# Performance work log

Hardware: AMD Instinct MI355X
Metric: run time of the kernel (lower is better)

The kernel has to match this reference:

```python
import jax, jax.numpy as jnp
import numpy as np

N, E, D_IN, D_H, D_OUT = 50000, 800000, 128, 128, 40
EPS = 1e-5


def setup_inputs() -> dict:
    key = jax.random.key(0)
    ks = jax.random.split(key, 12)
    x = jax.random.normal(ks[0], (N, D_IN), dtype=jnp.float32)
    edge_index = jax.random.randint(ks[1], (2, E), 0, N, dtype=jnp.int32)
    s = 1.0 / np.sqrt(D_H)
    return {
        "x": x,
        "edge_index": edge_index,
        "W1": jax.random.normal(ks[2], (D_IN, D_H), jnp.float32) * s,
        "b1": jnp.zeros((D_H,), jnp.float32),
        "W2": jax.random.normal(ks[3], (D_H, D_H), jnp.float32) * s,
        "b2": jnp.zeros((D_H,), jnp.float32),
        "g1": jnp.ones((D_H,), jnp.float32),
        "be1": jnp.zeros((D_H,), jnp.float32),
        "g2": jnp.ones((D_H,), jnp.float32),
        "be2": jnp.zeros((D_H,), jnp.float32),
        "g3": jnp.ones((D_H,), jnp.float32),
        "be3": jnp.zeros((D_H,), jnp.float32),
        "Wm": jax.random.normal(ks[4], (D_H, D_OUT), jnp.float32) * s,
        "bm": jnp.zeros((D_OUT,), jnp.float32),
    }


def _gcn_conv(x, W, b, src, dst, dinv):
    # GCNConv: x' = D^{-1/2}(A+I)D^{-1/2} (x W) + b
    xw = x @ W                                   # [N, H]
    coef = dinv[src] * dinv[dst]                 # [E]
    agg = jax.ops.segment_sum(xw[src] * coef[:, None], dst, num_segments=x.shape[0])
    agg = agg + xw * (dinv * dinv)[:, None]      # self-loop term
    return agg + b


def _bn(x, g, b):
    # BatchNorm1d in training mode: biased batch statistics over nodes
    m = jnp.mean(x, axis=0)
    v = jnp.var(x, axis=0)
    return g * (x - m) * jax.lax.rsqrt(v + EPS) + b


def reference(x, edge_index, W1, b1, W2, b2, g1, be1, g2, be2, g3, be3, Wm, bm):
    src, dst = edge_index[0], edge_index[1]
    # degree with self-loops (GCN symmetric normalization, computed on dst/col)
    deg = 1.0 + jax.ops.segment_sum(jnp.ones((E,), jnp.float32), dst, num_segments=N)
    dinv = jax.lax.rsqrt(deg)
    h = _gcn_conv(x, W1, b1, src, dst, dinv)
    h = jax.nn.relu(_bn(h, g1, be1))            # dropout is identity in eval
    h = _gcn_conv(h, W2, b2, src, dst, dinv)
    h = jax.nn.relu(_bn(h, g2, be2))
    h = _bn(h, g3, be3)
    h = h @ Wm + bm
    return jax.nn.log_softmax(h, axis=1)
```

## Files before the change

kernel.cpp:

```cpp
#include <hip/hip_runtime.h>
#include <hip/hip_fp16.h>
#include <math.h>

#define BN_EPS 1e-5f
#define CAP 128

typedef __attribute__((ext_vector_type(8))) short short8;
typedef __attribute__((ext_vector_type(4))) float floatx4;

__device__ inline unsigned short f2bf(float f) {
    union { float f; unsigned u; } x; x.f = f;
    unsigned r = x.u + 0x7fff + ((x.u >> 16) & 1);
    return (unsigned short)(r >> 16);
}
__device__ inline float bf2f(unsigned short h) {
    union { float f; unsigned u; } x; x.u = ((unsigned)h) << 16; return x.f;
}

__device__ inline void bn_sc_sh(float sum, float sumsq, float g, float be, float invN,
                                float& sc, float& sh) {
    float mean = sum * invN;
    float var = sumsq * invN - mean * mean;
    sc = g * rsqrtf(var + BN_EPS);
    sh = be - mean * sc;
}

__device__ inline void pack_one(int idx, const float* W1, const float* W2, const float* Wm,
                                unsigned short* p1, unsigned short* p2, unsigned short* pm) {
    const float* W;
    unsigned short* pack;
    int f, l = idx & 63, t, n, stride, ncols;
    if (idx < 2048) {
        W = W1; pack = p1; f = idx >> 6; t = f >> 3; n = (f & 7) * 16 + (l & 15);
        stride = 128; ncols = 128;
    } else if (idx < 4096) {
        W = W2; pack = p2; f = (idx - 2048) >> 6; t = f >> 3; n = (f & 7) * 16 + (l & 15);
        stride = 128; ncols = 128;
    } else {
        W = Wm; pack = pm; f = (idx - 4096) >> 6; t = f / 3; n = (f % 3) * 16 + (l & 15);
        stride = 40; ncols = 40;
    }
    int q = l >> 4;
    unsigned short* pp = pack + f * 1024 + l * 16;
#pragma unroll
    for (int j = 0; j < 8; ++j) {
        int k = t * 32 + q * 8 + j;
        float v = (n < ncols) ? W[k * stride + n] : 0.f;
        unsigned short hi = f2bf(v);
        float lo = v - bf2f(hi);
        pp[j] = hi;
        pp[8 + j] = f2bf(lo);
    }
}

__global__ __launch_bounds__(256) void k_pre(const float* __restrict__ W1,
                                             const float* __restrict__ W2,
                                             const float* __restrict__ Wm,
                                             unsigned short* __restrict__ p1,
                                             unsigned short* __restrict__ p2,
                                             unsigned short* __restrict__ pm,
                                             int4* __restrict__ zdst, int nz4) {
    if (blockIdx.x < 19) {
        int idx = blockIdx.x * 256 + threadIdx.x;
        if (idx < 4864) pack_one(idx, W1, W2, Wm, p1, p2, pm);
        return;
    }
    int i = (blockIdx.x - 19) * 256 + threadIdx.x;
    if (i < nz4) zdst[i] = make_int4(0, 0, 0, 0);
}

__global__ __launch_bounds__(256) void k_fill(const int* __restrict__ src,
                                              const int* __restrict__ dst, int E,
                                              int* __restrict__ fillc,
                                              unsigned short* __restrict__ col16, int nfill) {
    int b = (int)blockIdx.x;
    int g = b & 7;
    int rank = b >> 3;
    int stride = (nfill >> 3) * 256;
    for (int e = rank * 256 + threadIdx.x; e < E; e += stride) {
        int d = dst[e];
        if ((d & 7) != g) continue;
        int r = atomicAdd(&fillc[d], 1);
        if (r < CAP) col16[(size_t)d * CAP + r] = (unsigned short)src[e];
    }
}

__device__ inline void load_row8(const float* arow, int kbase, float av[8]) {
    float4 a0 = *(const float4*)(arow + kbase);
    float4 a1 = *(const float4*)(arow + kbase + 4);
    av[0] = a0.x; av[1] = a0.y; av[2] = a0.z; av[3] = a0.w;
    av[4] = a1.x; av[5] = a1.y; av[6] = a1.z; av[7] = a1.w;
}
__device__ inline void load_row8(const __half* arow, int kbase, float av[8]) {
    float4 raw = *(const float4*)(arow + kbase);
    const __half2* h = (const __half2*)&raw;
#pragma unroll
    for (int i = 0; i < 4; ++i) {
        float2 f = __half22float2(h[i]);
        av[2 * i] = f.x;
        av[2 * i + 1] = f.y;
    }
}

template <typename T, bool FUSE_BN>
__global__ __launch_bounds__(256) void k_gemm(const T* __restrict__ A,
                                              const unsigned short* __restrict__ packW,
                                              const float* __restrict__ sums,
                                              const float* __restrict__ g,
                                              const float* __restrict__ be, float invN,
                                              const int* __restrict__ fillc,
                                              __half* __restrict__ C16, int M) {
    int lane = threadIdx.x & 63;
    int wv = threadIdx.x >> 6;
    int m0 = ((int)blockIdx.x * 4 + wv) * 16;
    if (m0 >= M) return;
    int row = lane & 15, quad = lane >> 4;

    floatx4 acc[8];
#pragma unroll
    for (int nt = 0; nt < 8; ++nt) acc[nt] = (floatx4){0.f, 0.f, 0.f, 0.f};

    const T* arow = A + (size_t)(m0 + row) * 128;

    float av[4][8];
#pragma unroll
    for (int t = 0; t < 4; ++t) load_row8(arow, t * 32 + quad * 8, av[t]);

#pragma unroll
    for (int t = 0; t < 4; ++t) {
        int kbase = t * 32 + quad * 8;
        if (FUSE_BN) {
#pragma unroll
            for (int j = 0; j < 8; ++j) {
                int c = kbase + j;
                float sc, sh;
                bn_sc_sh(sums[c], sums[128 + c], g[c], be[c], invN, sc, sh);
                av[t][j] = fmaxf(av[t][j] * sc + sh, 0.f);
            }
        }
        short8 ah, al;
#pragma unroll
        for (int j = 0; j < 8; ++j) {
            unsigned short hi = f2bf(av[t][j]);
            ah[j] = (short)hi;
            al[j] = (short)f2bf(av[t][j] - bf2f(hi));
        }
        const unsigned short* wp = packW + (size_t)(t * 8) * 1024 + lane * 16;
#pragma unroll
        for (int nt = 0; nt < 8; ++nt) {
            short8 wh = *(const short8*)wp;
            short8 wl = *(const short8*)(wp + 8);
            wp += 1024;
            acc[nt] = __builtin_amdgcn_mfma_f32_16x16x32_bf16(ah, wh, acc[nt], 0, 0, 0);
            acc[nt] = __builtin_amdgcn_mfma_f32_16x16x32_bf16(al, wh, acc[nt], 0, 0, 0);
            acc[nt] = __builtin_amdgcn_mfma_f32_16x16x32_bf16(ah, wl, acc[nt], 0, 0, 0);
        }
    }

    float d[4];
#pragma unroll
    for (int r = 0; r < 4; ++r) d[r] = rsqrtf(1.f + (float)fillc[m0 + quad * 4 + r]);
#pragma unroll
    for (int nt = 0; nt < 8; ++nt) {
#pragma unroll
        for (int r = 0; r < 4; ++r) {
            C16[(size_t)(m0 + quad * 4 + r) * 128 + nt * 16 + row] =
                __float2half_rn(acc[nt][r] * d[r]);
        }
    }
}

__global__ __launch_bounds__(256) void k_gather(const __half2* __restrict__ y16,
                                                const int* __restrict__ fillc,
                                                const unsigned short* __restrict__ col16,
                                                const float* __restrict__ bias,
                                                __half2* __restrict__ out, int N) {
    int wv = threadIdx.x >> 6;
    int lane = threadIdx.x & 63;
    int n = blockIdx.x * 4 + wv;
    if (n >= N) return;
    float2 acc = __half22float2(y16[(size_t)n * 64 + lane]);
    int degraw = fillc[n];
    int deg = min(degraw, CAP);
    const unsigned short* cb = col16 + (size_t)n * CAP;
    for (int jb = 0; jb < deg; jb += 64) {
        int cnt = min(64, deg - jb);
        int idx = (lane < cnt) ? (int)cb[jb + lane] : 0;
        int jj = 0;
        for (; jj + 8 <= cnt; jj += 8) {
            int s0 = __shfl(idx, jj + 0, 64);
            int s1 = __shfl(idx, jj + 1, 64);
            int s2 = __shfl(idx, jj + 2, 64);
            int s3 = __shfl(idx, jj + 3, 64);
            int s4 = __shfl(idx, jj + 4, 64);
            int s5 = __shfl(idx, jj + 5, 64);
            int s6 = __shfl(idx, jj + 6, 64);
            int s7 = __shfl(idx, jj + 7, 64);
            float2 r0 = __half22float2(y16[(size_t)s0 * 64 + lane]);
            float2 r1 = __half22float2(y16[(size_t)s1 * 64 + lane]);
            float2 r2 = __half22float2(y16[(size_t)s2 * 64 + lane]);
            float2 r3 = __half22float2(y16[(size_t)s3 * 64 + lane]);
            float2 r4 = __half22float2(y16[(size_t)s4 * 64 + lane]);
            float2 r5 = __half22float2(y16[(size_t)s5 * 64 + lane]);
            float2 r6 = __half22float2(y16[(size_t)s6 * 64 + lane]);
            float2 r7 = __half22float2(y16[(size_t)s7 * 64 + lane]);
            acc.x += ((r0.x + r1.x) + (r2.x + r3.x)) + ((r4.x + r5.x) + (r6.x + r7.x));
            acc.y += ((r0.y + r1.y) + (r2.y + r3.y)) + ((r4.y + r5.y) + (r6.y + r7.y));
        }
        for (; jj < cnt; ++jj) {
            int s = __shfl(idx, jj, 64);
            float2 r = __half22float2(y16[(size_t)s * 64 + lane]);
            acc.x += r.x;
            acc.y += r.y;
        }
    }
    float dn = rsqrtf(1.f + (float)degraw);
    float2 b = *(const float2*)&bias[lane << 1];
    float2 o;
    o.x = dn * acc.x + b.x;
    o.y = dn * acc.y + b.y;
    out[(size_t)n * 64 + lane] = __float22half2_rn(o);
}

template <bool TRANSFORM>
__global__ __launch_bounds__(256) void k_stats(const __half2* __restrict__ h, int N,
                                               const float* __restrict__ sums2,
                                               const float* __restrict__ g2,
                                               const float* __restrict__ be2, float invN,
                                               float* __restrict__ stats) {
    int cp = threadIdx.x & 63;
    int rg = threadIdx.x >> 6;
    int rbeg = blockIdx.x * 256;
    int rend = min(rbeg + 256, N);
    float scx = 1.f, shx = 0.f, scy = 1.f, shy = 0.f;
    if (TRANSFORM) {
        int c = cp * 2;
        bn_sc_sh(sums2[c], sums2[128 + c], g2[c], be2[c], invN, scx, shx);
        bn_sc_sh(sums2[c + 1], sums2[128 + c + 1], g2[c + 1], be2[c + 1], invN, scy, shy);
    }
    float sx = 0.f, sy = 0.f, s2x = 0.f, s2y = 0.f;
    for (int r = rbeg + rg; r < rend; r += 4) {
        float2 v = __half22float2(h[(size_t)r * 64 + cp]);
        if (TRANSFORM) {
            v.x = fmaxf(v.x * scx + shx, 0.f);
            v.y = fmaxf(v.y * scy + shy, 0.f);
        }
        sx += v.x; sy += v.y;
        s2x += v.x * v.x; s2y += v.y * v.y;
    }
    __shared__ float ls[4][256];
    ls[0][threadIdx.x] = sx;
    ls[1][threadIdx.x] = sy;
    ls[2][threadIdx.x] = s2x;
    ls[3][threadIdx.x] = s2y;
    __syncthreads();
    if (threadIdx.x < 64) {
        int t = threadIdx.x;
        float a0 = ls[0][t] + ls[0][t + 64] + ls[0][t + 128] + ls[0][t + 192];
        float a1 = ls[1][t] + ls[1][t + 64] + ls[1][t + 128] + ls[1][t + 192];
        float a2 = ls[2][t] + ls[2][t + 64] + ls[2][t + 128] + ls[2][t + 192];
        float a3 = ls[3][t] + ls[3][t + 64] + ls[3][t + 128] + ls[3][t + 192];
        atomicAdd(&stats[2 * t], a0);
        atomicAdd(&stats[2 * t + 1], a1);
        atomicAdd(&stats[128 + 2 * t], a2);
        atomicAdd(&stats[128 + 2 * t + 1], a3);
    }
}

__global__ __launch_bounds__(256) void k_final(const __half* __restrict__ h,
                                               const float* __restrict__ sums2,
                                               const float* __restrict__ g2,
                                               const float* __restrict__ be2,
                                               const float* __restrict__ sums3,
                                               const float* __restrict__ g3,
                                               const float* __restrict__ be3, float invN,
                                               const unsigned short* __restrict__ packWm,
                                               const float* __restrict__ bm,
                                               float* __restrict__ out, int N) {
    int lane = threadIdx.x & 63;
    int wv = threadIdx.x >> 6;
    int m0 = ((int)blockIdx.x * 4 + wv) * 16;
    if (m0 >= N) return;
    int row = lane & 15, quad = lane >> 4;

    floatx4 acc[3];
#pragma unroll
    for (int nt = 0; nt < 3; ++nt) acc[nt] = (floatx4){0.f, 0.f, 0.f, 0.f};

    const __half* arow = h + (size_t)(m0 + row) * 128;

    float av[4][8];
#pragma unroll
    for (int t = 0; t < 4; ++t) load_row8(arow, t * 32 + quad * 8, av[t]);

#pragma unroll
    for (int t = 0; t < 4; ++t) {
        int kbase = t * 32 + quad * 8;
#pragma unroll
        for (int j = 0; j < 8; ++j) {
            int c = kbase + j;
            float sc2, sh2, sc3, sh3;
            bn_sc_sh(sums2[c], sums2[128 + c], g2[c], be2[c], invN, sc2, sh2);
            bn_sc_sh(sums3[c], sums3[128 + c], g3[c], be3[c], invN, sc3, sh3);
            av[t][j] = fmaxf(av[t][j] * sc2 + sh2, 0.f) * sc3 + sh3;
        }
        short8 ah, al;
#pragma unroll
        for (int j = 0; j < 8; ++j) {
            unsigned short hi = f2bf(av[t][j]);
            ah[j] = (short)hi;
            al[j] = (short)f2bf(av[t][j] - bf2f(hi));
        }
        const unsigned short* wp = packWm + (size_t)(t * 3) * 1024 + lane * 16;
#pragma unroll
        for (int nt = 0; nt < 3; ++nt) {
            short8 wh = *(const short8*)wp;
            short8 wl = *(const short8*)(wp + 8);
            wp += 1024;
            acc[nt] = __builtin_amdgcn_mfma_f32_16x16x32_bf16(ah, wh, acc[nt], 0, 0, 0);
            acc[nt] = __builtin_amdgcn_mfma_f32_16x16x32_bf16(al, wh, acc[nt], 0, 0, 0);
            acc[nt] = __builtin_amdgcn_mfma_f32_16x16x32_bf16(ah, wl, acc[nt], 0, 0, 0);
        }
    }

    float bb[3];
#pragma unroll
    for (int nt = 0; nt < 3; ++nt) {
        int col = nt * 16 + row;
        bb[nt] = (col < 40) ? bm[col] : 0.f;
    }
    bool val2 = (row < 8);

#pragma unroll
    for (int r = 0; r < 4; ++r) {
        int m = m0 + quad * 4 + r;
        float v0 = acc[0][r] + bb[0];
        float v1 = acc[1][r] + bb[1];
        float v2 = acc[2][r] + bb[2];
        float mx = fmaxf(v0, v1);
        if (val2) mx = fmaxf(mx, v2);
#pragma unroll
        for (int off = 1; off <= 8; off <<= 1) mx = fmaxf(mx, __shfl_xor(mx, off, 64));
        float s = expf(v0 - mx) + expf(v1 - mx) + (val2 ? expf(v2 - mx) : 0.f);
#pragma unroll
        for (int off = 1; off <= 8; off <<= 1) s += __shfl_xor(s, off, 64);
        float lse = mx + logf(s);
        if (m < N) {
            out[(size_t)m * 40 + row] = v0 - lse;
            out[(size_t)m * 40 + 16 + row] = v1 - lse;
            if (val2) out[(size_t)m * 40 + 32 + row] = v2 - lse;
        }
    }
}

extern "C" void kernel_launch(void* const* d_in, const int* in_sizes, int n_in,
                              void* d_out, int out_size, void* d_ws, size_t ws_size,
                              hipStream_t stream) {
    const float* x   = (const float*)d_in[0];
    const int*   ei  = (const int*)d_in[1];
    const float* W1  = (const float*)d_in[2];
    const float* b1  = (const float*)d_in[3];
    const float* W2  = (const float*)d_in[4];
    const float* b2  = (const float*)d_in[5];
    const float* g1  = (const float*)d_in[6];
    const float* be1 = (const float*)d_in[7];
    const float* g2  = (const float*)d_in[8];
    const float* be2 = (const float*)d_in[9];
    const float* g3  = (const float*)d_in[10];
    const float* be3 = (const float*)d_in[11];
    const float* Wm  = (const float*)d_in[12];
    const float* bm  = (const float*)d_in[13];
    float* out = (float*)d_out;

    int N = in_sizes[0] / 128;
    int E = in_sizes[1] / 2;
    const int* srcs = ei;
    const int* dsts = ei + E;
    float invN = 1.0f / (float)N;

    char* ws = (char*)d_ws;
    size_t off = 0;
    auto alloc = [&](size_t bytes) -> void* {
        void* p = ws + off;
        off += (bytes + 255) & ~(size_t)255;
        return p;
    };
    size_t fill_rounded = (((size_t)N * 4) + 255) & ~(size_t)255;
    int*   fillc   = (int*)alloc((size_t)N * 4);
    float* statsAll= (float*)alloc(3 * 256 * 4);
    float* stats1  = statsAll;
    float* stats2  = statsAll + 256;
    float* stats3  = statsAll + 512;
    unsigned short* col16 = (unsigned short*)alloc((size_t)N * CAP * 2);
    unsigned short* packW1 = (unsigned short*)alloc(32768 * 2);
    unsigned short* packW2 = (unsigned short*)alloc(32768 * 2);
    unsigned short* packWm = (unsigned short*)alloc(12288 * 2);
    __half* y16 = (__half*)alloc((size_t)N * 128 * 2);
    __half* h16 = (__half*)alloc((size_t)N * 128 * 2);
    (void)ws_size; (void)n_in; (void)out_size;

    int nthb = (N + 255) / 256;
    int gatherb = (N + 3) / 4;
    int ngemm = (N + 63) / 64;
    int gfb = (N + 63) / 64;
    const int NFILL = 8192;

    int nz4 = (int)((fill_rounded + 3 * 256 * 4) / 16);
    int zb = (nz4 + 255) / 256;

    k_pre<<<19 + zb, 256, 0, stream>>>(W1, W2, Wm, packW1, packW2, packWm,
                                       (int4*)fillc, nz4);

    k_fill<<<NFILL, 256, 0, stream>>>(srcs, dsts, E, fillc, col16, NFILL);

    k_gemm<float, false><<<ngemm, 256, 0, stream>>>(x, packW1, nullptr, nullptr, nullptr,
                                                    invN, fillc, y16, N);
    k_gather<<<gatherb, 256, 0, stream>>>((const __half2*)y16, fillc, col16, b1,
                                          (__half2*)h16, N);
    k_stats<false><<<nthb, 256, 0, stream>>>((const __half2*)h16, N, nullptr, nullptr, nullptr,
                                             invN, stats1);

    k_gemm<__half, true><<<ngemm, 256, 0, stream>>>(h16, packW2, stats1, g1, be1, invN,
                                                    fillc, y16, N);
    k_gather<<<gatherb, 256, 0, stream>>>((const __half2*)y16, fillc, col16, b2,
                                          (__half2*)h16, N);
    k_stats<false><<<nthb, 256, 0, stream>>>((const __half2*)h16, N, nullptr, nullptr, nullptr,
                                             invN, stats2);

    k_stats<true><<<nthb, 256, 0, stream>>>((const __half2*)h16, N, stats2, g2, be2, invN,
                                            stats3);
    k_final<<<gfb, 256, 0, stream>>>(h16, stats2, g2, be2, stats3, g3, be3, invN, packWm, bm,
                                     out, N);
}
```

Baseline: 322.0 us.

## Merge prep/fill and gather/stats phases into cooperative kernels with grid sync

Replaces separate launches for weight packing plus zeroing plus CSR fill, and for gather plus batch-norm statistics, with persistent cooperative kernels that use grid-wide syncs between phases. The aim is to cut kernel launch gaps and tail effects. In exchange the grid is limited to occupancy-sized persistent blocks, the per-block stats reduction covers more rows, and the fill loses its dst-modulo grouping, which may change atomic contention. Non-cooperative fallbacks are kept.

```diff
diff --git a/kernel.cpp b/kernel.cpp
--- a/kernel.cpp
+++ b/kernel.cpp
@@ -1,6 +1,9 @@
 #include <hip/hip_runtime.h>
+#include <hip/hip_cooperative_groups.h>
 #include <hip/hip_fp16.h>
 #include <math.h>
+
+namespace cg = cooperative_groups;
 
 #define BN_EPS 1e-5f
 #define CAP 128
@@ -53,38 +56,6 @@
     }
 }
 
-__global__ __launch_bounds__(256) void k_pre(const float* __restrict__ W1,
-                                             const float* __restrict__ W2,
-                                             const float* __restrict__ Wm,
-                                             unsigned short* __restrict__ p1,
-                                             unsigned short* __restrict__ p2,
-                                             unsigned short* __restrict__ pm,
-                                             int4* __restrict__ zdst, int nz4) {
-    if (blockIdx.x < 19) {
-        int idx = blockIdx.x * 256 + threadIdx.x;
-        if (idx < 4864) pack_one(idx, W1, W2, Wm, p1, p2, pm);
-        return;
-    }
-    int i = (blockIdx.x - 19) * 256 + threadIdx.x;
-    if (i < nz4) zdst[i] = make_int4(0, 0, 0, 0);
-}
-
-__global__ __launch_bounds__(256) void k_fill(const int* __restrict__ src,
-                                              const int* __restrict__ dst, int E,
-                                              int* __restrict__ fillc,
-                                              unsigned short* __restrict__ col16, int nfill) {
-    int b = (int)blockIdx.x;
-    int g = b & 7;
-    int rank = b >> 3;
-    int stride = (nfill >> 3) * 256;
-    for (int e = rank * 256 + threadIdx.x; e < E; e += stride) {
-        int d = dst[e];
-        if ((d & 7) != g) continue;
-        int r = atomicAdd(&fillc[d], 1);
-        if (r < CAP) col16[(size_t)d * CAP + r] = (unsigned short)src[e];
-    }
-}
-
 __device__ inline void load_row8(const float* arow, int kbase, float av[8]) {
     float4 a0 = *(const float4*)(arow + kbase);
     float4 a1 = *(const float4*)(arow + kbase + 4);
@@ -170,68 +141,67 @@
     }
 }
 
-__global__ __launch_bounds__(256) void k_gather(const __half2* __restrict__ y16,
-                                                const int* __restrict__ fillc,
-                                                const unsigned short* __restrict__ col16,
-                                                const float* __restrict__ bias,
-                                                __half2* __restrict__ out, int N) {
+__device__ void gather_body(const __half2* __restrict__ y16, const int* __restrict__ fillc,
+                            const unsigned short* __restrict__ col16,
+                            const float* __restrict__ bias, __half2* __restrict__ out,
+                            int N) {
     int wv = threadIdx.x >> 6;
     int lane = threadIdx.x & 63;
-    int n = blockIdx.x * 4 + wv;
-    if (n >= N) return;
-    float2 acc = __half22float2(y16[(size_t)n * 64 + lane]);
-    int degraw = fillc[n];
-    int deg = min(degraw, CAP);
-    const unsigned short* cb = col16 + (size_t)n * CAP;
-    for (int jb = 0; jb < deg; jb += 64) {
-        int cnt = min(64, deg - jb);
-        int idx = (lane < cnt) ? (int)cb[jb + lane] : 0;
-        int jj = 0;
-        for (; jj + 8 <= cnt; jj += 8) {
-            int s0 = __shfl(idx, jj + 0, 64);
-            int s1 = __shfl(idx, jj + 1, 64);
-            int s2 = __shfl(idx, jj + 2, 64);
-            int s3 = __shfl(idx, jj + 3, 64);
-            int s4 = __shfl(idx, jj + 4, 64);
-            int s5 = __shfl(idx, jj + 5, 64);
-            int s6 = __shfl(idx, jj + 6, 64);
-            int s7 = __shfl(idx, jj + 7, 64);
-            float2 r0 = __half22float2(y16[(size_t)s0 * 64 + lane]);
-            float2 r1 = __half22float2(y16[(size_t)s1 * 64 + lane]);
-            float2 r2 = __half22float2(y16[(size_t)s2 * 64 + lane]);
-            float2 r3 = __half22float2(y16[(size_t)s3 * 64 + lane]);
-            float2 r4 = __half22float2(y16[(size_t)s4 * 64 + lane]);
-            float2 r5 = __half22float2(y16[(size_t)s5 * 64 + lane]);
-            float2 r6 = __half22float2(y16[(size_t)s6 * 64 + lane]);
-            float2 r7 = __half22float2(y16[(size_t)s7 * 64 + lane]);
-            acc.x += ((r0.x + r1.x) + (r2.x + r3.x)) + ((r4.x + r5.x) + (r6.x + r7.x));
-            acc.y += ((r0.y + r1.y) + (r2.y + r3.y)) + ((r4.y + r5.y) + (r6.y + r7.y));
-        }
-        for (; jj < cnt; ++jj) {
-            int s = __shfl(idx, jj, 64);
-            float2 r = __half22float2(y16[(size_t)s * 64 + lane]);
-            acc.x += r.x;
-            acc.y += r.y;
-        }
-    }
-    float dn = rsqrtf(1.f + (float)degraw);
+    int nwave = (int)gridDim.x * 4;
     float2 b = *(const float2*)&bias[lane << 1];
-    float2 o;
-    o.x = dn * acc.x + b.x;
-    o.y = dn * acc.y + b.y;
-    out[(size_t)n * 64 + lane] = __float22half2_rn(o);
+    for (int n = (int)blockIdx.x * 4 + wv; n < N; n += nwave) {
+        float2 acc = __half22float2(y16[(size_t)n * 64 + lane]);
+        int degraw = fillc[n];
+        int deg = min(degraw, CAP);
+        const unsigned short* cb = col16 + (size_t)n * CAP;
+        for (int jb = 0; jb < deg; jb += 64) {
+            int cnt = min(64, deg - jb);
+            int idx = (lane < cnt) ? (int)cb[jb + lane] : 0;
+            int jj = 0;
+            for (; jj + 8 <= cnt; jj += 8) {
+                int s0 = __shfl(idx, jj + 0, 64);
+                int s1 = __shfl(idx, jj + 1, 64);
+                int s2 = __shfl(idx, jj + 2, 64);
+                int s3 = __shfl(idx, jj + 3, 64);
+                int s4 = __shfl(idx, jj + 4, 64);
+                int s5 = __shfl(idx, jj + 5, 64);
+                int s6 = __shfl(idx, jj + 6, 64);
+                int s7 = __shfl(idx, jj + 7, 64);
+                float2 r0 = __half22float2(y16[(size_t)s0 * 64 + lane]);
+                float2 r1 = __half22float2(y16[(size_t)s1 * 64 + lane]);
+                float2 r2 = __half22float2(y16[(size_t)s2 * 64 + lane]);
+                float2 r3 = __half22float2(y16[(size_t)s3 * 64 + lane]);
+                float2 r4 = __half22float2(y16[(size_t)s4 * 64 + lane]);
+                float2 r5 = __half22float2(y16[(size_t)s5 * 64 + lane]);
+                float2 r6 = __half22float2(y16[(size_t)s6 * 64 + lane]);
+                float2 r7 = __half22float2(y16[(size_t)s7 * 64 + lane]);
+                acc.x += ((r0.x + r1.x) + (r2.x + r3.x)) + ((r4.x + r5.x) + (r6.x + r7.x));
+                acc.y += ((r0.y + r1.y) + (r2.y + r3.y)) + ((r4.y + r5.y) + (r6.y + r7.y));
+            }
+            for (; jj < cnt; ++jj) {
+                int s = __shfl(idx, jj, 64);
+                float2 r = __half22float2(y16[(size_t)s * 64 + lane]);
+                acc.x += r.x;
+                acc.y += r.y;
+            }
+        }
+        float dn = rsqrtf(1.f + (float)degraw);
+        float2 o;
+        o.x = dn * acc.x + b.x;
+        o.y = dn * acc.y + b.y;
+        out[(size_t)n * 64 + lane] = __float22half2_rn(o);
+    }
 }
 
 template <bool TRANSFORM>
-__global__ __launch_bounds__(256) void k_stats(const __half2* __restrict__ h, int N,
-                                               const float* __restrict__ sums2,
-                                               const float* __restrict__ g2,
-                                               const float* __restrict__ be2, float invN,
-                                               float* __restrict__ stats) {
+__device__ void stats_body(const __half2* __restrict__ h, int N,
+                           const float* __restrict__ sums2, const float* __restrict__ g2,
+                           const float* __restrict__ be2, float invN,
+                           float* __restrict__ stats, float (&ls)[4][256]) {
+    int nchunk = (N + 255) >> 8;
+    if ((int)blockIdx.x >= nchunk) return;
     int cp = threadIdx.x & 63;
     int rg = threadIdx.x >> 6;
-    int rbeg = blockIdx.x * 256;
-    int rend = min(rbeg + 256, N);
     float scx = 1.f, shx = 0.f, scy = 1.f, shy = 0.f;
     if (TRANSFORM) {
         int c = cp * 2;
@@ -239,16 +209,18 @@
         bn_sc_sh(sums2[c + 1], sums2[128 + c + 1], g2[c + 1], be2[c + 1], invN, scy, shy);
     }
     float sx = 0.f, sy = 0.f, s2x = 0.f, s2y = 0.f;
-    for (int r = rbeg + rg; r < rend; r += 4) {
-        float2 v = __half22float2(h[(size_t)r * 64 + cp]);
-        if (TRANSFORM) {
-            v.x = fmaxf(v.x * scx + shx, 0.f);
-            v.y = fmaxf(v.y * scy + shy, 0.f);
-        }
-        sx += v.x; sy += v.y;
-        s2x += v.x * v.x; s2y += v.y * v.y;
-    }
-    __shared__ float ls[4][256];
+    for (int r0 = (int)blockIdx.x * 256; r0 < N; r0 += (int)gridDim.x * 256) {
+        int rend = min(r0 + 256, N);
+        for (int r = r0 + rg; r < rend; r += 4) {
+            float2 v = __half22float2(h[(size_t)r * 64 + cp]);
+            if (TRANSFORM) {
+                v.x = fmaxf(v.x * scx + shx, 0.f);
+                v.y = fmaxf(v.y * scy + shy, 0.f);
+            }
+            sx += v.x; sy += v.y;
+            s2x += v.x * v.x; s2y += v.y * v.y;
+        }
+    }
     ls[0][threadIdx.x] = sx;
     ls[1][threadIdx.x] = sy;
     ls[2][threadIdx.x] = s2x;
@@ -265,6 +237,109 @@
         atomicAdd(&stats[128 + 2 * t], a2);
         atomicAdd(&stats[128 + 2 * t + 1], a3);
     }
+    __syncthreads();
+}
+
+__global__ __launch_bounds__(256) void k_prep(const float* __restrict__ W1,
+                                              const float* __restrict__ W2,
+                                              const float* __restrict__ Wm,
+                                              unsigned short* __restrict__ p1,
+                                              unsigned short* __restrict__ p2,
+                                              unsigned short* __restrict__ pm,
+                                              int4* __restrict__ z, int nz4,
+                                              const int* __restrict__ src,
+                                              const int* __restrict__ dst, int E,
+                                              int* __restrict__ fillc,
+                                              unsigned short* __restrict__ col16) {
+    cg::grid_group gg = cg::this_grid();
+    int gtid = (int)blockIdx.x * 256 + threadIdx.x;
+    int nthr = (int)gridDim.x * 256;
+    if (gtid < 4864) pack_one(gtid, W1, W2, Wm, p1, p2, pm);
+    for (int i = gtid; i < nz4; i += nthr) z[i] = make_int4(0, 0, 0, 0);
+    gg.sync();
+    for (int e = gtid; e < E; e += nthr) {
+        int d = dst[e];
+        int r = atomicAdd(&fillc[d], 1);
+        if (r < CAP) col16[(size_t)d * CAP + r] = (unsigned short)src[e];
+    }
+}
+
+__global__ __launch_bounds__(256) void k_gs1(const __half2* __restrict__ y16,
+                                             const int* __restrict__ fillc,
+                                             const unsigned short* __restrict__ col16,
+                                             const float* __restrict__ bias,
+                                             __half2* __restrict__ out, int N,
+                                             float* __restrict__ stats1) {
+    cg::grid_group gg = cg::this_grid();
+    __shared__ float ls[4][256];
+    gather_body(y16, fillc, col16, bias, out, N);
+    gg.sync();
+    stats_body<false>(out, N, nullptr, nullptr, nullptr, 0.f, stats1, ls);
+}
+
+__global__ __launch_bounds__(256) void k_gs2(const __half2* __restrict__ y16,
+                                             const int* __restrict__ fillc,
+                                             const unsigned short* __restrict__ col16,
+                                             const float* __restrict__ bias,
+                                             __half2* __restrict__ out, int N,
+                                             float* __restrict__ stats2,
+                                             const float* __restrict__ g2,
+                                             const float* __restrict__ be2, float invN,
+                                             float* __restrict__ stats3) {
+    cg::grid_group gg = cg::this_grid();
+    __shared__ float ls[4][256];
+    gather_body(y16, fillc, col16, bias, out, N);
+    gg.sync();
+    stats_body<false>(out, N, nullptr, nullptr, nullptr, 0.f, stats2, ls);
+    gg.sync();
+    stats_body<true>(out, N, stats2, g2, be2, invN, stats3, ls);
+}
+
+__global__ __launch_bounds__(256) void k_pre(const float* __restrict__ W1,
+                                             const float* __restrict__ W2,
+                                             const float* __restrict__ Wm,
+                                             unsigned short* __restrict__ p1,
+                                             unsigned short* __restrict__ p2,
+                                             unsigned short* __restrict__ pm,
+                                             int4* __restrict__ zdst, int nz4) {
+    if (blockIdx.x < 19) {
+        int idx = blockIdx.x * 256 + threadIdx.x;
+        if (idx < 4864) pack_one(idx, W1, W2, Wm, p1, p2, pm);
+        return;
+    }
+    int i = ((int)blockIdx.x - 19) * 256 + threadIdx.x;
+    if (i < nz4) zdst[i] = make_int4(0, 0, 0, 0);
+}
+
+__global__ __launch_bounds__(256) void k_fill(const int* __restrict__ src,
+                                              const int* __restrict__ dst, int E,
+                                              int* __restrict__ fillc,
+                                              unsigned short* __restrict__ col16) {
+    int gtid = (int)blockIdx.x * 256 + threadIdx.x;
+    int nthr = (int)gridDim.x * 256;
+    for (int e = gtid; e < E; e += nthr) {
+        int d = dst[e];
+        int r = atomicAdd(&fillc[d], 1);
+        if (r < CAP) col16[(size_t)d * CAP + r] = (unsigned short)src[e];
+    }
+}
+
+__global__ __launch_bounds__(256) void k_gather(const __half2* __restrict__ y16,
+                                                const int* __restrict__ fillc,
+                                                const unsigned short* __restrict__ col16,
+                                                const float* __restrict__ bias,
+                                                __half2* __restrict__ out, int N) {
+    gather_body(y16, fillc, col16, bias, out, N);
+}
+
+template <bool TRANSFORM>
+__global__ __launch_bounds__(256) void k_stats(const __half2* __restrict__ h, int N,
+                                               const float* __restrict__ sums2,
+                                               const float* __restrict__ g2,
+                                               const float* __restrict__ be2, float invN,
+                                               float* __restrict__ stats) {
+    __shared__ float ls[4][256];
+    stats_body<TRANSFORM>(h, N, sums2, g2, be2, invN, stats, ls);
 }
 
 __global__ __launch_bounds__(256) void k_final(const __half* __restrict__ h,
@@ -399,36 +474,85 @@
     __half* h16 = (__half*)alloc((size_t)N * 128 * 2);
     (void)ws_size; (void)n_in; (void)out_size;
 
+    int nz4 = (int)((fill_rounded + 3 * 256 * 4) / 16);
+    int ngemm = (N + 63) / 64;
+    int gatherb = (N + 3) / 4;
     int nthb = (N + 255) / 256;
-    int gatherb = (N + 3) / 4;
-    int ngemm = (N + 63) / 64;
-    int gfb = (N + 63) / 64;
-    const int NFILL = 8192;
-
-    int nz4 = (int)((fill_rounded + 3 * 256 * 4) / 16);
-    int zb = (nz4 + 255) / 256;
-
-    k_pre<<<19 + zb, 256, 0, stream>>>(W1, W2, Wm, packW1, packW2, packWm,
-                                       (int4*)fillc, nz4);
-
-    k_fill<<<NFILL, 256, 0, stream>>>(srcs, dsts, E, fillc, col16, NFILL);
+
+    auto coop_grid = [&](const void* f) -> int {
+        int mb = 0;
+        if (hipOccupancyMaxActiveBlocksPerMultiprocessor(&mb, f, 256, 0) != hipSuccess)
+            return 0;
+        if (mb < 1) return 0;
+        if (mb > 8) mb = 8;
+        return mb * 256;
+    };
+
+    {
+        int grid = coop_grid((const void*)k_prep);
+        bool done = false;
+        if (grid > 0) {
+            void* ka[] = {(void*)&W1, (void*)&W2, (void*)&Wm, (void*)&packW1, (void*)&packW2,
+                          (void*)&packWm, (void*)&fillc, (void*)&nz4, (void*)&srcs,
+                          (void*)&dsts, (void*)&E, (void*)&fillc, (void*)&col16};
+            done = hipLaunchCooperativeKernel((const void*)k_prep, dim3(grid), dim3(256), ka,
+                                              0, stream) == hipSuccess;
+        }
+        if (!done) {
+            int zb = (nz4 + 255) / 256;
+            k_pre<<<19 + zb, 256, 0, stream>>>(W1, W2, Wm, packW1, packW2, packWm,
+                                               (int4*)fillc, nz4);
+            k_fill<<<2048, 256, 0, stream>>>(srcs, dsts, E, fillc, col16);
+        }
+    }
 
     k_gemm<float, false><<<ngemm, 256, 0, stream>>>(x, packW1, nullptr, nullptr, nullptr,
                                                     invN, fillc, y16, N);
-    k_gather<<<gatherb, 256, 0, stream>>>((const __half2*)y16, fillc, col16, b1,
-                                          (__half2*)h16, N);
-    k_stats<false><<<nthb, 256, 0, stream>>>((const __half2*)h16, N, nullptr, nullptr, nullptr,
-                                             invN, stats1);
+
+    {
+        int grid = coop_grid((const void*)k_gs1);
+        bool done = false;
+        if (grid > 0) {
+            const __half2* yp = (const __half2*)y16;
+            __half2* hp = (__half2*)h16;
+            void* ka[] = {(void*)&yp, (void*)&fillc, (void*)&col16, (void*)&b1, (void*)&hp,
+                          (void*)&N, (void*)&stats1};
+            done = hipLaunchCooperativeKernel((const void*)k_gs1, dim3(grid), dim3(256), ka,
+                                              0, stream) == hipSuccess;
+        }
+        if (!done) {
+            k_gather<<<gatherb, 256, 0, stream>>>((const __half2*)y16, fillc, col16, b1,
+                                                  (__half2*)h16, N);
+            k_stats<false><<<nthb, 256, 0, stream>>>((const __half2*)h16, N, nullptr,
+                                                     nullptr, nullptr, invN, stats1);
+        }
+    }
 
     k_gemm<__half, true><<<ngemm, 256, 0, stream>>>(h16, packW2, stats1, g1, be1, invN,
                                                     fillc, y16, N);
-    k_gather<<<gatherb, 256, 0, stream>>>((const __half2*)y16, fillc, col16, b2,
-                                          (__half2*)h16, N);
-    k_stats<false><<<nthb, 256, 0, stream>>>((const __half2*)h16, N, nullptr, nullptr, nullptr,
-                                             invN, stats2);
-
-    k_stats<true><<<nthb, 256, 0, stream>>>((const __half2*)h16, N, stats2, g2, be2, invN,
-                                            stats3);
-    k_final<<<gfb, 256, 0, stream>>>(h16, stats2, g2, be2, stats3, g3, be3, invN, packWm, bm,
-                                     out, N);
-}
+
+    {
+        int grid = coop_grid((const void*)k_gs2);
+        bool done = false;
+        if (grid > 0) {
+            const __half2* yp = (const __half2*)y16;
+            __half2* hp = (__half2*)h16;
+            void* ka[] = {(void*)&yp, (void*)&fillc, (void*)&col16, (void*)&b2, (void*)&hp,
+                          (void*)&N, (void*)&stats2, (void*)&g2, (void*)&be2, (void*)&invN,
+                          (void*)&stats3};
+            done = hipLaunchCooperativeKernel((const void*)k_gs2, dim3(grid), dim3(256), ka,
+                                              0, stream) == hipSuccess;
+        }
+        if (!done) {
+            k_gather<<<gatherb, 256, 0, stream>>>((const __half2*)y16, fillc, col16, b2,
+                                                  (__half2*)h16, N);
+            k_stats<false><<<nthb, 256, 0, stream>>>((const __half2*)h16, N, nullptr,
+                                                     nullptr, nullptr, invN, stats2);
+            k_stats<true><<<nthb, 256, 0, stream>>>((const __half2*)h16, N, stats2, g2, be2,
+                                                    invN, stats3);
+        }
+    }
+
+    k_final<<<ngemm, 256, 0, stream>>>(h16, stats2, g2, be2, stats3, g3, be3, invN, packWm,
+                                       bm, out, N);
+}
```

Measured after the change: 1.005 ms. 3.12x slower.
